# Kernel tuning notes

Hardware: AMD Instinct MI355X
Metric: run time of the kernel (lower is better)

## Reference

```python
import jax, jax.numpy as jnp
import numpy as np

L, B, S, D, H, DK, F = 6, 4, 2048, 512, 8, 64, 2048


def setup_inputs() -> dict:
    key = jax.random.key(0)
    ks = iter(jax.random.split(key, 40))
    def rn(shape, scale=0.02):
        return jax.random.normal(next(ks), shape, jnp.float32) * scale
    inp = {
        "x": jax.random.normal(next(ks), (B, S, D), jnp.float32),
        "enc": jax.random.normal(next(ks), (B, S, D), jnp.float32),
    }
    for pre in ("sa", "ca"):
        inp[f"{pre}_wq"] = rn((L, D, H * DK)); inp[f"{pre}_bq"] = jnp.zeros((L, H * DK), jnp.float32)
        inp[f"{pre}_wk"] = rn((L, D, H * DK)); inp[f"{pre}_bk"] = jnp.zeros((L, H * DK), jnp.float32)
        inp[f"{pre}_wv"] = rn((L, D, H * DK)); inp[f"{pre}_bv"] = jnp.zeros((L, H * DK), jnp.float32)
        inp[f"{pre}_wo"] = rn((L, H * DK, D)); inp[f"{pre}_bo"] = jnp.zeros((L, D), jnp.float32)
    for i in (1, 2, 3):
        inp[f"ln{i}_g"] = jnp.ones((L, D), jnp.float32)
        inp[f"ln{i}_b"] = jnp.zeros((L, D), jnp.float32)
    inp["ff_w1"] = rn((L, D, F)); inp["ff_b1"] = jnp.zeros((L, F), jnp.float32)
    inp["ff_w2"] = rn((L, F, D)); inp["ff_b2"] = jnp.zeros((L, D), jnp.float32)
    return inp


def _layer_norm(z, g, b, eps=1e-5):
    m = z.mean(-1, keepdims=True)
    v = z.var(-1, keepdims=True)
    return (z - m) * jax.lax.rsqrt(v + eps) * g + b


def _mha(q_in, kv_in, wq, bq, wk, bk, wv, bv, wo, bo, causal_bias):
    b, s, _ = q_in.shape
    Q = (q_in @ wq + bq).reshape(b, s, H, DK)   # [B,S,H,DK]
    K = (kv_in @ wk + bk).reshape(b, s, H, DK)
    V = (kv_in @ wv + bv).reshape(b, s, H, DK)
    scores = jnp.einsum("bqhd,bkhd->bhqk", Q, K) / jnp.float32(DK) ** 0.5
    if causal_bias is not None:
        scores = scores + causal_bias  # additive -inf above diagonal
    w = jax.nn.softmax(scores, axis=-1)
    att = jnp.einsum("bhqk,bkhd->bqhd", w, V).reshape(b, s, H * DK)
    return att @ wo + bo


def reference(x, enc, sa_wq, sa_bq, sa_wk, sa_bk, sa_wv, sa_bv, sa_wo, sa_bo,
              ca_wq, ca_bq, ca_wk, ca_bk, ca_wv, ca_bv, ca_wo, ca_bo,
              ln1_g, ln1_b, ln2_g, ln2_b, ln3_g, ln3_b,
              ff_w1, ff_b1, ff_w2, ff_b2):
    s = x.shape[1]
    causal_bias = jnp.triu(jnp.full((s, s), -jnp.inf, jnp.float32), 1)

    params = (sa_wq, sa_bq, sa_wk, sa_bk, sa_wv, sa_bv, sa_wo, sa_bo,
              ca_wq, ca_bq, ca_wk, ca_bk, ca_wv, ca_bv, ca_wo, ca_bo,
              ln1_g, ln1_b, ln2_g, ln2_b, ln3_g, ln3_b,
              ff_w1, ff_b1, ff_w2, ff_b2)

    def block(h, p):
        (swq, sbq, swk, sbk, swv, sbv, swo, sbo,
         cwq, cbq, cwk, cbk, cwv, cbv, cwo, cbo,
         g1, b1, g2, b2, g3, b3, w1, bb1, w2, bb2) = p
        # masked self-attention + residual + LN  (faithful to source)
        x1 = _layer_norm(h + _mha(h, h, swq, sbq, swk, sbk, swv, sbv, swo, sbo, causal_bias), g1, b1)
        # cross-attention; residual comes from the BLOCK INPUT h (source bug kept)
        y = _layer_norm(h + _mha(x1, enc, cwq, cbq, cwk, cbk, cwv, cbv, cwo, cbo, None), g2, b2)
        # FFN; residual from x1 (source bug kept)
        out = _layer_norm(x1 + (jax.nn.relu(y @ w1 + bb1) @ w2 + bb2), g3, b3)
        return out, None

    out, _ = jax.lax.scan(block, x, params)
    return out
```

## Files before the change

### kernel.cpp

```cpp
#include <hip/hip_runtime.h>
#include <stdint.h>

#define LCOUNT 6
#define BB 4
#define SS 2048
#define DD 512
#define HH 8
#define DKK 64
#define FFDIM 2048
#define MM (BB*SS)

typedef __attribute__((ext_vector_type(8))) __bf16 bf16x8;
typedef __attribute__((ext_vector_type(4))) float f32x4;
typedef unsigned short u16;
typedef unsigned long long u64;

__device__ __forceinline__ u16 f2bf(float f) {
  union { __bf16 h; u16 u; } v; v.h = (__bf16)f; return v.u;
}
__device__ __forceinline__ float bf2f(u16 u) {
  union { uint32_t u; float f; } v; v.u = ((uint32_t)u) << 16;
  return v.f;
}

__device__ __forceinline__ void gload_lds16(const u16* gsrc, u16* ldst) {
  __builtin_amdgcn_global_load_lds((const __attribute__((address_space(1))) char*)gsrc,
                                   (__attribute__((address_space(3))) char*)ldst, 16, 0, 0);
}

__global__ __launch_bounds__(256) void f2bf_kernel(const float* __restrict__ in,
                                                   u16* __restrict__ outp, int n) {
  int i = (blockIdx.x * 256 + threadIdx.x) * 8;
  if (i >= n) return;
  float4 a = *(const float4*)&in[i];
  float4 b = *(const float4*)&in[i + 4];
  union { u16 us[8]; uint4 v; } pk;
  pk.us[0] = f2bf(a.x); pk.us[1] = f2bf(a.y); pk.us[2] = f2bf(a.z); pk.us[3] = f2bf(a.w);
  pk.us[4] = f2bf(b.x); pk.us[5] = f2bf(b.y); pk.us[6] = f2bf(b.z); pk.us[7] = f2bf(b.w);
  *(uint4*)&outp[i] = pk.v;
}

__global__ __launch_bounds__(256) void bias_cat(const float* a, const float* b, const float* c,
                                                float* dst, int n, int total) {
  int i = blockIdx.x * 256 + threadIdx.x;
  if (i >= total) return;
  int parts = (c != nullptr) ? 3 : 2;
  int per = parts * n;
  int l = i / per, cc = i % per;
  const float* s = cc < n ? a : (cc < 2 * n ? b : c);
  dst[i] = s[l * n + (cc % n)];
}

__global__ __launch_bounds__(256) void wtrans(const float* __restrict__ W,
                                              u16* __restrict__ Wt, int K_, int N_,
                                              size_t lstride) {
  __shared__ float tile[64 * 65];
  const int l = blockIdx.z;
  const float* Wl = W + (size_t)l * K_ * N_;
  u16* Wtl = Wt + (size_t)l * lstride;
  const int n0 = blockIdx.x * 64, k0 = blockIdx.y * 64;
  const int tid = threadIdx.x;
  const int r = tid >> 2, c4 = (tid & 3) * 16;
#pragma unroll
  for (int j = 0; j < 16; j += 4) {
    float4 v = *(const float4*)&Wl[(size_t)(k0 + r) * N_ + n0 + c4 + j];
    tile[r * 65 + c4 + j + 0] = v.x;
    tile[r * 65 + c4 + j + 1] = v.y;
    tile[r * 65 + c4 + j + 2] = v.z;
    tile[r * 65 + c4 + j + 3] = v.w;
  }
  __syncthreads();
  const int nr = tid >> 2, kc = (tid & 3) * 16;
#pragma unroll
  for (int half = 0; half < 2; ++half) {
    union { u16 us[8]; uint4 v; } pk;
#pragma unroll
    for (int e = 0; e < 8; ++e) pk.us[e] = f2bf(tile[(kc + half * 8 + e) * 65 + nr]);
    *(uint4*)&Wtl[(size_t)(n0 + nr) * K_ + k0 + kc + half * 8] = pk.v;
  }
}

template <int BMT, int BNT, int BKT, bool RELU, bool VT>
__global__ __launch_bounds__(256)
void gemm_bt(const u16* __restrict__ A, const u16* __restrict__ Bt,
             const float* __restrict__ bias, u16* __restrict__ C,
             int N_, int K_, int CS, u16* __restrict__ vt, int vtc0) {
  constexpr int MR = BMT / 32;
  constexpr int NR = BNT / 32;
  constexpr int CH = BKT / 8;
  constexpr int RPR = 2048 / BKT;
  constexpr int KS = BKT / 32;
  __shared__ u16 As[BMT * BKT];
  __shared__ u16 Bs[BNT * BKT];
  const int tid = threadIdx.x;
  const int wid = tid >> 6, lane = tid & 63;
  const int l15 = lane & 15, g = lane >> 4;
  const int wr = wid >> 1, wc = wid & 1;
  const int lrow = (CH == 8) ? (lane >> 3) : (lane >> 4);
  const int lch  = lane & (CH - 1);
  const int wrows = 64 / CH;
  const int lin = blockIdx.x + gridDim.x * blockIdx.y;
  const int nwg = gridDim.x * gridDim.y;
  const int swz = (lin & 7) * (nwg >> 3) + (lin >> 3);
  const int brow = (swz / gridDim.x) * BMT;
  const int bcol = (swz % gridDim.x) * BNT;

  f32x4 acc[MR][NR];
#pragma unroll
  for (int m = 0; m < MR; ++m)
#pragma unroll
    for (int n = 0; n < NR; ++n) acc[m][n] = (f32x4){0.f, 0.f, 0.f, 0.f};

  for (int kt = 0; kt < K_; kt += BKT) {
#pragma unroll
    for (int r = 0; r < BMT / RPR; ++r) {
      int row = r * RPR + wid * wrows + lrow;
      int slot = lch ^ (row & 7);
      gload_lds16(A + (size_t)(brow + row) * K_ + kt + slot * 8,
                  &As[r * 2048 + wid * 512]);
    }
#pragma unroll
    for (int r = 0; r < BNT / RPR; ++r) {
      int row = r * RPR + wid * wrows + lrow;
      int slot = lch ^ (row & 7);
      gload_lds16(Bt + (size_t)(bcol + row) * K_ + kt + slot * 8,
                  &Bs[r * 2048 + wid * 512]);
    }
    __syncthreads();
#pragma unroll
    for (int ks = 0; ks < KS; ++ks) {
      bf16x8 af[MR], bfr[NR];
#pragma unroll
      for (int m = 0; m < MR; ++m) {
        int row = wr * (BMT / 2) + m * 16 + l15;
        int slot = (ks * 4 + g) ^ (row & 7);
        af[m] = *(const bf16x8*)&As[row * BKT + slot * 8];
      }
#pragma unroll
      for (int n = 0; n < NR; ++n) {
        int row = wc * (BNT / 2) + n * 16 + l15;
        int slot = (ks * 4 + g) ^ (row & 7);
        bfr[n] = *(const bf16x8*)&Bs[row * BKT + slot * 8];
      }
#pragma unroll
      for (int m = 0; m < MR; ++m)
#pragma unroll
        for (int n = 0; n < NR; ++n)
          acc[m][n] = __builtin_amdgcn_mfma_f32_16x16x32_bf16(af[m], bfr[n], acc[m][n], 0, 0, 0);
    }
    __syncthreads();
  }
#pragma unroll
  for (int n = 0; n < NR; ++n) {
    int col = bcol + wc * (BNT / 2) + n * 16 + l15;
    float bv = bias ? bias[col] : 0.f;
    if (VT && col >= vtc0) {
      int hh = (col - vtc0) >> 6, dd = (col - vtc0) & 63;
#pragma unroll
      for (int m = 0; m < MR; ++m) {
        int s0g = brow + wr * (BMT / 2) + m * 16 + g * 4;
        int bb = s0g >> 11, ss = s0g & (SS - 1);
        union { u16 us[4]; uint2 v; } pk;
#pragma unroll
        for (int r = 0; r < 4; ++r) pk.us[r] = f2bf(acc[m][n][r] + bv);
        *(uint2*)&vt[(((size_t)(bb * HH + hh)) * DKK + dd) * SS + ss] = pk.v;
      }
    } else {
#pragma unroll
      for (int m = 0; m < MR; ++m) {
#pragma unroll
        for (int r = 0; r < 4; ++r) {
          int rowg = brow + wr * (BMT / 2) + m * 16 + g * 4 + r;
          float v = acc[m][n][r] + bv;
          if (RELU) v = fmaxf(v, 0.f);
          C[(size_t)rowg * CS + col] = f2bf(v);
        }
      }
    }
  }
}

template <bool CAUSAL>
__global__ __launch_bounds__(256, 4)
void attn_kernel(const u16* __restrict__ Qm, const u16* __restrict__ Km,
                 const u16* __restrict__ Vt, u16* __restrict__ Om, int qks) {
  __shared__ u16 Ks[2][64 * 64];
  __shared__ u16 Vs[2][64 * 64];
  const int lin = blockIdx.x;
  const int bh = (lin & 7) * 4 + ((lin >> 3) >> 5);
  const int qc = (lin >> 3) & 31;
  const int qb = (qc & 1) ? (31 - (qc >> 1)) : (qc >> 1);
  const int h = bh & 7, b = bh >> 3;
  const int tid = threadIdx.x, wid = tid >> 6, lane = tid & 63;
  const int l15 = lane & 15, g = lane >> 4;
  const int qstart = qb * 64;
  const size_t qbase = ((size_t)b * SS) * qks + h * DKK;
  const size_t vtbase = (size_t)(b * HH + h) * DKK * SS;
  const size_t obase = ((size_t)b * SS) * DD + h * DKK;
  const int srow = wid * 8 + (lane >> 3);
  const int sslot = lane & 7;
  const int qg = qstart + wid * 16 + l15;
  const float SC = 0.18033688f;
  const int sA = ((2 * g) & 3) * 16 + l15;
  const int sB = ((2 * g + 1) & 3) * 16 + l15;

  const u16* kp = Km + qbase;
  const u16* vp = Vt + vtbase;

  bf16x8 qf[2];
#pragma unroll
  for (int ks = 0; ks < 2; ++ks)
    qf[ks] = *(const bf16x8*)&Qm[qbase + (size_t)qg * qks + ks * 32 + g * 8];

  f32x4 oacc[4];
#pragma unroll
  for (int nb = 0; nb < 4; ++nb) oacc[nb] = (f32x4){0.f, 0.f, 0.f, 0.f};
  float m_run = -3.0e38f, l_run = 0.f;

  const int T = CAUSAL ? (qb + 1) : (SS / 64);

#pragma unroll
  for (int r = 0; r < 2; ++r) {
    int row = r * 32 + srow;
    int slot = sslot ^ (row & 7);
    gload_lds16(kp + (size_t)row * qks + slot * 8, &Ks[0][r * 2048 + wid * 512]);
    gload_lds16(vp + (size_t)row * SS + slot * 8, &Vs[0][r * 2048 + wid * 512]);
  }
  __syncthreads();

  int cur = 0;
  for (int t = 0; t < T; ++t) {
    const int kstart = t * 64;
    if (t + 1 < T) {
#pragma unroll
      for (int r = 0; r < 2; ++r) {
        int row = r * 32 + srow;
        int slot = sslot ^ (row & 7);
        gload_lds16(kp + (size_t)(kstart + 64 + row) * qks + slot * 8,
                    &Ks[cur ^ 1][r * 2048 + wid * 512]);
        gload_lds16(vp + (size_t)row * SS + kstart + 64 + slot * 8,
                    &Vs[cur ^ 1][r * 2048 + wid * 512]);
      }
    }
    f32x4 sacc[4];
#pragma unroll
    for (int nb = 0; nb < 4; ++nb) sacc[nb] = (f32x4){0.f, 0.f, 0.f, 0.f};
    __builtin_amdgcn_s_setprio(1);
#pragma unroll
    for (int nb = 0; nb < 4; ++nb) {
      int row = nb * 16 + l15;
#pragma unroll
      for (int ks = 0; ks < 2; ++ks) {
        bf16x8 kf = *(const bf16x8*)&Ks[cur][row * 64 + (((ks * 4 + g) ^ (row & 7)) * 8)];
        sacc[nb] = __builtin_amdgcn_mfma_f32_16x16x32_bf16(kf, qf[ks], sacc[nb], 0, 0, 0);
      }
    }
    __builtin_amdgcn_s_setprio(0);
    if (CAUSAL && t == T - 1) {
#pragma unroll
      for (int nb = 0; nb < 4; ++nb)
#pragma unroll
        for (int r = 0; r < 4; ++r)
          if ((kstart + nb * 16 + g * 4 + r) > qg) sacc[nb][r] = -3.0e38f;
    }
    f32x4 m4 = sacc[0];
#pragma unroll
    for (int nb = 1; nb < 4; ++nb) {
      m4[0] = fmaxf(m4[0], sacc[nb][0]); m4[1] = fmaxf(m4[1], sacc[nb][1]);
      m4[2] = fmaxf(m4[2], sacc[nb][2]); m4[3] = fmaxf(m4[3], sacc[nb][3]);
    }
    float mx = fmaxf(fmaxf(m4[0], m4[1]), fmaxf(m4[2], m4[3]));
    mx = fmaxf(mx, __shfl_xor(mx, 16));
    mx = fmaxf(mx, __shfl_xor(mx, 32));
    const bool skip = __all(mx <= m_run + 64.0f);
    float mnew = skip ? m_run : fmaxf(m_run, mx);
    float mc = mnew * SC;
    float s = 0.f;
#pragma unroll
    for (int nb = 0; nb < 4; ++nb) {
#pragma unroll
      for (int r = 0; r < 4; ++r) {
        float e = __builtin_amdgcn_exp2f(sacc[nb][r] * SC - mc);
        sacc[nb][r] = e; s += e;
      }
    }
    s += __shfl_xor(s, 16);
    s += __shfl_xor(s, 32);
    if (skip) {
      l_run += s;
    } else {
      float resc = __builtin_amdgcn_exp2f((m_run - mnew) * SC);
      l_run = l_run * resc + s;
      m_run = mnew;
      float ro[4];
#pragma unroll
      for (int r = 0; r < 4; ++r) ro[r] = __shfl(resc, g * 4 + r);
#pragma unroll
      for (int nb = 0; nb < 4; ++nb)
#pragma unroll
        for (int r = 0; r < 4; ++r) oacc[nb][r] *= ro[r];
    }
    u64 pk[4];
#pragma unroll
    for (int nb = 0; nb < 4; ++nb) {
      union { u16 us[4]; u64 v; } z;
#pragma unroll
      for (int r = 0; r < 4; ++r) z.us[r] = f2bf(sacc[nb][r]);
      pk[nb] = z.v;
    }
    bf16x8 pf[2];
#pragma unroll
    for (int ks = 0; ks < 2; ++ks) {
      u64 a0 = __shfl(pk[2 * ks], sA);
      u64 a1 = __shfl(pk[2 * ks + 1], sA);
      u64 b0 = __shfl(pk[2 * ks], sB);
      u64 b1 = __shfl(pk[2 * ks + 1], sB);
      union { u64 q[2]; bf16x8 v; } mrg;
      mrg.q[0] = (g < 2) ? a0 : a1;
      mrg.q[1] = (g < 2) ? b0 : b1;
      pf[ks] = mrg.v;
    }
    __builtin_amdgcn_s_setprio(1);
#pragma unroll
    for (int nb = 0; nb < 4; ++nb) {
      int row = nb * 16 + l15;
#pragma unroll
      for (int ks = 0; ks < 2; ++ks) {
        bf16x8 vf = *(const bf16x8*)&Vs[cur][row * 64 + (((ks * 4 + g) ^ (row & 7)) * 8)];
        oacc[nb] = __builtin_amdgcn_mfma_f32_16x16x32_bf16(pf[ks], vf, oacc[nb], 0, 0, 0);
      }
    }
    __builtin_amdgcn_s_setprio(0);
    __syncthreads();
    cur ^= 1;
  }
  float linv = 1.f / l_run;
  float io[4];
#pragma unroll
  for (int r = 0; r < 4; ++r) io[r] = __shfl(linv, g * 4 + r);
#pragma unroll
  for (int nb = 0; nb < 4; ++nb) {
#pragma unroll
    for (int r = 0; r < 4; ++r) {
      Om[obase + (size_t)(qstart + wid * 16 + g * 4 + r) * DD + nb * 16 + l15] =
          f2bf(oacc[nb][r] * io[r]);
    }
  }
}

__global__ __launch_bounds__(256)
void ln_kernel(const u16* __restrict__ A, const u16* __restrict__ Bv,
               const float* __restrict__ gamma, const float* __restrict__ beta,
               u16* __restrict__ out_bf, float* __restrict__ out_f32) {
  const int row = blockIdx.x * 4 + (threadIdx.x >> 6);
  const int lane = threadIdx.x & 63;
  uint4 av = *(const uint4*)&A[(size_t)row * DD + lane * 8];
  uint4 bv = *(const uint4*)&Bv[(size_t)row * DD + lane * 8];
  const u16* au = (const u16*)&av;
  const u16* bu = (const u16*)&bv;
  float z[8], s = 0.f, s2 = 0.f;
#pragma unroll
  for (int j = 0; j < 8; ++j) {
    float x = bf2f(au[j]) + bf2f(bu[j]);
    z[j] = x; s += x; s2 += x * x;
  }
#pragma unroll
  for (int off = 1; off < 64; off <<= 1) {
    s += __shfl_xor(s, off);
    s2 += __shfl_xor(s2, off);
  }
  float mean = s * (1.f / 512.f);
  float var = s2 * (1.f / 512.f) - mean * mean;
  float rs = rsqrtf(var + 1e-5f);
  union { u16 us[8]; uint4 v; } pk;
#pragma unroll
  for (int j = 0; j < 8; ++j) {
    float o = (z[j] - mean) * rs * gamma[lane * 8 + j] + beta[lane * 8 + j];
    pk.us[j] = f2bf(o);
    if (out_f32) out_f32[(size_t)row * DD + lane * 8 + j] = o;
  }
  *(uint4*)&out_bf[(size_t)row * DD + lane * 8] = pk.v;
}

extern "C" void kernel_launch(void* const* d_in, const int* in_sizes, int n_in,
                              void* d_out, int out_size, void* d_ws, size_t ws_size,
                              hipStream_t stream) {
  const float* x   = (const float*)d_in[0];
  const float* enc = (const float*)d_in[1];
  const float* sa_w[4] = {(const float*)d_in[2], (const float*)d_in[4], (const float*)d_in[6], (const float*)d_in[8]};
  const float* sa_b[4] = {(const float*)d_in[3], (const float*)d_in[5], (const float*)d_in[7], (const float*)d_in[9]};
  const float* ca_w[4] = {(const float*)d_in[10], (const float*)d_in[12], (const float*)d_in[14], (const float*)d_in[16]};
  const float* ca_b[4] = {(const float*)d_in[11], (const float*)d_in[13], (const float*)d_in[15], (const float*)d_in[17]};
  const float* ln_g[3] = {(const float*)d_in[18], (const float*)d_in[20], (const float*)d_in[22]};
  const float* ln_b[3] = {(const float*)d_in[19], (const float*)d_in[21], (const float*)d_in[23]};
  const float* ffw1 = (const float*)d_in[24];
  const float* ffb1 = (const float*)d_in[25];
  const float* ffw2 = (const float*)d_in[26];
  const float* ffb2 = (const float*)d_in[27];

  char* ws = (char*)d_ws;
  size_t o = 0;
  auto take = [&](size_t bytes) {
    void* p = ws + o;
    o += (bytes + 255) & ~(size_t)255;
    return p;
  };
  u16* wqkv  = (u16*)take((size_t)LCOUNT * 1536 * 512 * 2);
  u16* wqca  = (u16*)take((size_t)LCOUNT * 512 * 512 * 2);
  u16* wkvca = (u16*)take((size_t)LCOUNT * 1024 * 512 * 2);
  u16* wosa  = (u16*)take((size_t)LCOUNT * 512 * 512 * 2);
  u16* woca  = (u16*)take((size_t)LCOUNT * 512 * 512 * 2);
  u16* w1t   = (u16*)take((size_t)LCOUNT * 512 * 2048 * 2);
  u16* w2t   = (u16*)take((size_t)LCOUNT * 2048 * 512 * 2);
  float* bqkv = (float*)take((size_t)LCOUNT * 1536 * 4);
  float* bkv  = (float*)take((size_t)LCOUNT * 1024 * 4);
  u16* Hb   = (u16*)take((size_t)MM * 512 * 2);
  u16* Eb   = (u16*)take((size_t)MM * 512 * 2);
  u16* QKVb = (u16*)take((size_t)MM * 1536 * 2);
  u16* Ab   = (u16*)take((size_t)MM * 512 * 2);
  u16* Pb   = (u16*)take((size_t)MM * 512 * 2);
  u16* X1b  = (u16*)take((size_t)MM * 512 * 2);
  u16* Yb   = (u16*)take((size_t)MM * 512 * 2);
  u16* Fb   = (u16*)take((size_t)MM * 2048 * 2);
  u16* Vtb  = Fb;

  f2bf_kernel<<<2048, 256, 0, stream>>>(x, Hb, MM * 512);
  f2bf_kernel<<<2048, 256, 0, stream>>>(enc, Eb, MM * 512);
  wtrans<<<dim3(8, 8, LCOUNT), 256, 0, stream>>>(sa_w[0], wqkv,              512, 512, (size_t)1536 * 512);
  wtrans<<<dim3(8, 8, LCOUNT), 256, 0, stream>>>(sa_w[1], wqkv + 512 * 512,  512, 512, (size_t)1536 * 512);
  wtrans<<<dim3(8, 8, LCOUNT), 256, 0, stream>>>(sa_w[2], wqkv + 1024 * 512, 512, 512, (size_t)1536 * 512);
  wtrans<<<dim3(8, 8, LCOUNT), 256, 0, stream>>>(sa_w[3], wosa,              512, 512, (size_t)512 * 512);
  wtrans<<<dim3(8, 8, LCOUNT), 256, 0, stream>>>(ca_w[0], wqca,              512, 512, (size_t)512 * 512);
  wtrans<<<dim3(8, 8, LCOUNT), 256, 0, stream>>>(ca_w[1], wkvca,             512, 512, (size_t)1024 * 512);
  wtrans<<<dim3(8, 8, LCOUNT), 256, 0, stream>>>(ca_w[2], wkvca + 512 * 512, 512, 512, (size_t)1024 * 512);
  wtrans<<<dim3(8, 8, LCOUNT), 256, 0, stream>>>(ca_w[3], woca,              512, 512, (size_t)512 * 512);
  wtrans<<<dim3(32, 8, LCOUNT), 256, 0, stream>>>(ffw1, w1t, 512, 2048, (size_t)2048 * 512);
  wtrans<<<dim3(8, 32, LCOUNT), 256, 0, stream>>>(ffw2, w2t, 2048, 512, (size_t)512 * 2048);
  bias_cat<<<36, 256, 0, stream>>>(sa_b[0], sa_b[1], sa_b[2], bqkv, 512, LCOUNT * 1536);
  bias_cat<<<24, 256, 0, stream>>>(ca_b[1], ca_b[2], nullptr, bkv, 512, LCOUNT * 1024);

  for (int l = 0; l < LCOUNT; ++l) {
    const size_t w512 = (size_t)l * 512 * 512;
    const size_t wff = (size_t)l * 512 * 2048;
    gemm_bt<128, 128, 64, false, true><<<dim3(12, 64), 256, 0, stream>>>(
        Hb, wqkv + (size_t)l * 1536 * 512, bqkv + l * 1536, QKVb, 1536, 512, 1536, Vtb, 1024);
    attn_kernel<true><<<dim3(1024), 256, 0, stream>>>(QKVb, QKVb + 512, Vtb, Ab, 1536);
    gemm_bt<64, 64, 128, false, false><<<dim3(8, 128), 256, 0, stream>>>(
        Ab, wosa + w512, sa_b[3] + l * 512, Pb, 512, 512, 512, nullptr, 0);
    ln_kernel<<<MM / 4, 256, 0, stream>>>(Hb, Pb, ln_g[0] + l * 512, ln_b[0] + l * 512, X1b, nullptr);
    gemm_bt<64, 64, 128, false, false><<<dim3(8, 128), 256, 0, stream>>>(
        X1b, wqca + w512, ca_b[0] + l * 512, QKVb, 512, 512, 1536, nullptr, 0);
    gemm_bt<128, 128, 64, false, true><<<dim3(8, 64), 256, 0, stream>>>(
        Eb, wkvca + (size_t)l * 1024 * 512, bkv + l * 1024, QKVb + 512, 1024, 512, 1536, Vtb, 512);
    attn_kernel<false><<<dim3(1024), 256, 0, stream>>>(QKVb, QKVb + 512, Vtb, Ab, 1536);
    gemm_bt<64, 64, 128, false, false><<<dim3(8, 128), 256, 0, stream>>>(
        Ab, woca + w512, ca_b[3] + l * 512, Pb, 512, 512, 512, nullptr, 0);
    ln_kernel<<<MM / 4, 256, 0, stream>>>(Hb, Pb, ln_g[1] + l * 512, ln_b[1] + l * 512, Yb, nullptr);
    gemm_bt<128, 128, 64, true, false><<<dim3(16, 64), 256, 0, stream>>>(
        Yb, w1t + wff, ffb1 + l * 2048, Fb, 2048, 512, 2048, nullptr, 0);
    gemm_bt<64, 64, 128, false, false><<<dim3(8, 128), 256, 0, stream>>>(
        Fb, w2t + wff, ffb2 + l * 512, Pb, 512, 2048, 512, nullptr, 0);
    ln_kernel<<<MM / 4, 256, 0, stream>>>(X1b, Pb, ln_g[2] + l * 512, ln_b[2] + l * 512, Hb,
                                          (l == LCOUNT - 1) ? (float*)d_out : nullptr);
  }
}
```

Baseline: 2.040 ms.

## Fuse cross-attn Q/KV GEMMs, batch weight transposes, LDS P-relayout, wider N tiles

Cross-attention Q and KV projections become one 1536-wide GEMM launch, where column blocks at or past 512 read the encoder activations through a second A pointer. The eight 512x512 weight transposes are batched into a single launch. In attention, the P-matrix relayout now goes through a per-wave LDS scratch buffer instead of shuffles. The N=512 output GEMMs move from 64x64 to 64x128 tiles. Together these cut launch count and shuffle cost, at the price of extra LDS use in attention and fewer workgroups for the output GEMMs.

```diff
diff --git a/kernel.cpp b/kernel.cpp
--- a/kernel.cpp
+++ b/kernel.cpp
@@ -13,7 +13,6 @@
 typedef __attribute__((ext_vector_type(8))) __bf16 bf16x8;
 typedef __attribute__((ext_vector_type(4))) float f32x4;
 typedef unsigned short u16;
-typedef unsigned long long u64;
 
 __device__ __forceinline__ u16 f2bf(float f) {
   union { __bf16 h; u16 u; } v; v.h = (__bf16)f; return v.u;
@@ -80,11 +79,45 @@
   }
 }
 
+struct WtBatch {
+  const float* src[8];
+  u16* dst[8];
+  unsigned long long lstr[8];
+};
+__global__ __launch_bounds__(256) void wtrans8(WtBatch wb) {
+  __shared__ float tile[64 * 65];
+  const int z = blockIdx.z;
+  const int slot = z / 6, l = z - slot * 6;
+  const float* Wl = wb.src[slot] + (size_t)l * 512 * 512;
+  u16* Wtl = wb.dst[slot] + (size_t)l * wb.lstr[slot];
+  const int n0 = blockIdx.x * 64, k0 = blockIdx.y * 64;
+  const int tid = threadIdx.x;
+  const int r = tid >> 2, c4 = (tid & 3) * 16;
+#pragma unroll
+  for (int j = 0; j < 16; j += 4) {
+    float4 v = *(const float4*)&Wl[(size_t)(k0 + r) * 512 + n0 + c4 + j];
+    tile[r * 65 + c4 + j + 0] = v.x;
+    tile[r * 65 + c4 + j + 1] = v.y;
+    tile[r * 65 + c4 + j + 2] = v.z;
+    tile[r * 65 + c4 + j + 3] = v.w;
+  }
+  __syncthreads();
+  const int nr = tid >> 2, kc = (tid & 3) * 16;
+#pragma unroll
+  for (int half = 0; half < 2; ++half) {
+    union { u16 us[8]; uint4 v; } pk;
+#pragma unroll
+    for (int e = 0; e < 8; ++e) pk.us[e] = f2bf(tile[(kc + half * 8 + e) * 65 + nr]);
+    *(uint4*)&Wtl[(size_t)(n0 + nr) * 512 + k0 + kc + half * 8] = pk.v;
+  }
+}
+
 template <int BMT, int BNT, int BKT, bool RELU, bool VT>
 __global__ __launch_bounds__(256)
 void gemm_bt(const u16* __restrict__ A, const u16* __restrict__ Bt,
              const float* __restrict__ bias, u16* __restrict__ C,
-             int N_, int K_, int CS, u16* __restrict__ vt, int vtc0) {
+             int N_, int K_, int CS, u16* __restrict__ vt, int vtc0,
+             const u16* __restrict__ A2, int a2col) {
   constexpr int MR = BMT / 32;
   constexpr int NR = BNT / 32;
   constexpr int CH = BKT / 8;
@@ -104,6 +137,7 @@
   const int swz = (lin & 7) * (nwg >> 3) + (lin >> 3);
   const int brow = (swz / gridDim.x) * BMT;
   const int bcol = (swz % gridDim.x) * BNT;
+  const u16* Ap = (A2 != nullptr && bcol >= a2col) ? A2 : A;
 
   f32x4 acc[MR][NR];
 #pragma unroll
@@ -116,7 +150,7 @@
     for (int r = 0; r < BMT / RPR; ++r) {
       int row = r * RPR + wid * wrows + lrow;
       int slot = lch ^ (row & 7);
-      gload_lds16(A + (size_t)(brow + row) * K_ + kt + slot * 8,
+      gload_lds16(Ap + (size_t)(brow + row) * K_ + kt + slot * 8,
                   &As[r * 2048 + wid * 512]);
     }
 #pragma unroll
@@ -186,6 +220,7 @@
                  const u16* __restrict__ Vt, u16* __restrict__ Om, int qks) {
   __shared__ u16 Ks[2][64 * 64];
   __shared__ u16 Vs[2][64 * 64];
+  __shared__ u16 Ps[4][16 * 64];
   const int lin = blockIdx.x;
   const int bh = (lin & 7) * 4 + ((lin >> 3) >> 5);
   const int qc = (lin >> 3) & 31;
@@ -197,12 +232,12 @@
   const size_t qbase = ((size_t)b * SS) * qks + h * DKK;
   const size_t vtbase = (size_t)(b * HH + h) * DKK * SS;
   const size_t obase = ((size_t)b * SS) * DD + h * DKK;
+  u16* psw = &Ps[wid][0];
   const int srow = wid * 8 + (lane >> 3);
   const int sslot = lane & 7;
   const int qg = qstart + wid * 16 + l15;
+  const int pswz = (l15 & 7) << 1;
   const float SC = 0.18033688f;
-  const int sA = ((2 * g) & 3) * 16 + l15;
-  const int sB = ((2 * g + 1) & 3) * 16 + l15;
 
   const u16* kp = Km + qbase;
   const u16* vp = Vt + vtbase;
@@ -300,25 +335,19 @@
 #pragma unroll
         for (int r = 0; r < 4; ++r) oacc[nb][r] *= ro[r];
     }
-    u64 pk[4];
 #pragma unroll
     for (int nb = 0; nb < 4; ++nb) {
-      union { u16 us[4]; u64 v; } z;
-#pragma unroll
-      for (int r = 0; r < 4; ++r) z.us[r] = f2bf(sacc[nb][r]);
-      pk[nb] = z.v;
+      union { u16 us[4]; uint2 v; } pk;
+#pragma unroll
+      for (int r = 0; r < 4; ++r) pk.us[r] = f2bf(sacc[nb][r]);
+      int cp = (nb * 4 + g) ^ pswz;
+      *(uint2*)&psw[l15 * 64 + cp * 4] = pk.v;
     }
     bf16x8 pf[2];
 #pragma unroll
     for (int ks = 0; ks < 2; ++ks) {
-      u64 a0 = __shfl(pk[2 * ks], sA);
-      u64 a1 = __shfl(pk[2 * ks + 1], sA);
-      u64 b0 = __shfl(pk[2 * ks], sB);
-      u64 b1 = __shfl(pk[2 * ks + 1], sB);
-      union { u64 q[2]; bf16x8 v; } mrg;
-      mrg.q[0] = (g < 2) ? a0 : a1;
-      mrg.q[1] = (g < 2) ? b0 : b1;
-      pf[ks] = mrg.v;
+      int cp0 = (8 * ks + 2 * g) ^ pswz;
+      pf[ks] = *(const bf16x8*)&psw[l15 * 64 + cp0 * 4];
     }
     __builtin_amdgcn_s_setprio(1);
 #pragma unroll
@@ -406,14 +435,13 @@
     return p;
   };
   u16* wqkv  = (u16*)take((size_t)LCOUNT * 1536 * 512 * 2);
-  u16* wqca  = (u16*)take((size_t)LCOUNT * 512 * 512 * 2);
-  u16* wkvca = (u16*)take((size_t)LCOUNT * 1024 * 512 * 2);
+  u16* wca   = (u16*)take((size_t)LCOUNT * 1536 * 512 * 2);
   u16* wosa  = (u16*)take((size_t)LCOUNT * 512 * 512 * 2);
   u16* woca  = (u16*)take((size_t)LCOUNT * 512 * 512 * 2);
   u16* w1t   = (u16*)take((size_t)LCOUNT * 512 * 2048 * 2);
   u16* w2t   = (u16*)take((size_t)LCOUNT * 2048 * 512 * 2);
   float* bqkv = (float*)take((size_t)LCOUNT * 1536 * 4);
-  float* bkv  = (float*)take((size_t)LCOUNT * 1024 * 4);
+  float* bca  = (float*)take((size_t)LCOUNT * 1536 * 4);
   u16* Hb   = (u16*)take((size_t)MM * 512 * 2);
   u16* Eb   = (u16*)take((size_t)MM * 512 * 2);
   u16* QKVb = (u16*)take((size_t)MM * 1536 * 2);
@@ -426,40 +454,42 @@
 
   f2bf_kernel<<<2048, 256, 0, stream>>>(x, Hb, MM * 512);
   f2bf_kernel<<<2048, 256, 0, stream>>>(enc, Eb, MM * 512);
-  wtrans<<<dim3(8, 8, LCOUNT), 256, 0, stream>>>(sa_w[0], wqkv,              512, 512, (size_t)1536 * 512);
-  wtrans<<<dim3(8, 8, LCOUNT), 256, 0, stream>>>(sa_w[1], wqkv + 512 * 512,  512, 512, (size_t)1536 * 512);
-  wtrans<<<dim3(8, 8, LCOUNT), 256, 0, stream>>>(sa_w[2], wqkv + 1024 * 512, 512, 512, (size_t)1536 * 512);
-  wtrans<<<dim3(8, 8, LCOUNT), 256, 0, stream>>>(sa_w[3], wosa,              512, 512, (size_t)512 * 512);
-  wtrans<<<dim3(8, 8, LCOUNT), 256, 0, stream>>>(ca_w[0], wqca,              512, 512, (size_t)512 * 512);
-  wtrans<<<dim3(8, 8, LCOUNT), 256, 0, stream>>>(ca_w[1], wkvca,             512, 512, (size_t)1024 * 512);
-  wtrans<<<dim3(8, 8, LCOUNT), 256, 0, stream>>>(ca_w[2], wkvca + 512 * 512, 512, 512, (size_t)1024 * 512);
-  wtrans<<<dim3(8, 8, LCOUNT), 256, 0, stream>>>(ca_w[3], woca,              512, 512, (size_t)512 * 512);
+  WtBatch wb;
+  wb.src[0] = sa_w[0]; wb.dst[0] = wqkv;              wb.lstr[0] = (size_t)1536 * 512;
+  wb.src[1] = sa_w[1]; wb.dst[1] = wqkv + 512 * 512;  wb.lstr[1] = (size_t)1536 * 512;
+  wb.src[2] = sa_w[2]; wb.dst[2] = wqkv + 1024 * 512; wb.lstr[2] = (size_t)1536 * 512;
+  wb.src[3] = sa_w[3]; wb.dst[3] = wosa;              wb.lstr[3] = (size_t)512 * 512;
+  wb.src[4] = ca_w[0]; wb.dst[4] = wca;               wb.lstr[4] = (size_t)1536 * 512;
+  wb.src[5] = ca_w[1]; wb.dst[5] = wca + 512 * 512;   wb.lstr[5] = (size_t)1536 * 512;
+  wb.src[6] = ca_w[2]; wb.dst[6] = wca + 1024 * 512;  wb.lstr[6] = (size_t)1536 * 512;
+  wb.src[7] = ca_w[3]; wb.dst[7] = woca;              wb.lstr[7] = (size_t)512 * 512;
+  wtrans8<<<dim3(8, 8, 48), 256, 0, stream>>>(wb);
   wtrans<<<dim3(32, 8, LCOUNT), 256, 0, stream>>>(ffw1, w1t, 512, 2048, (size_t)2048 * 512);
   wtrans<<<dim3(8, 32, LCOUNT), 256, 0, stream>>>(ffw2, w2t, 2048, 512, (size_t)512 * 2048);
   bias_cat<<<36, 256, 0, stream>>>(sa_b[0], sa_b[1], sa_b[2], bqkv, 512, LCOUNT * 1536);
-  bias_cat<<<24, 256, 0, stream>>>(ca_b[1], ca_b[2], nullptr, bkv, 512, LCOUNT * 1024);
+  bias_cat<<<36, 256, 0, stream>>>(ca_b[0], ca_b[1], ca_b[2], bca, 512, LCOUNT * 1536);
 
   for (int l = 0; l < LCOUNT; ++l) {
     const size_t w512 = (size_t)l * 512 * 512;
     const size_t wff = (size_t)l * 512 * 2048;
     gemm_bt<128, 128, 64, false, true><<<dim3(12, 64), 256, 0, stream>>>(
-        Hb, wqkv + (size_t)l * 1536 * 512, bqkv + l * 1536, QKVb, 1536, 512, 1536, Vtb, 1024);
+        Hb, wqkv + (size_t)l * 1536 * 512, bqkv + l * 1536, QKVb, 1536, 512, 1536, Vtb, 1024,
+        nullptr, 0);
     attn_kernel<true><<<dim3(1024), 256, 0, stream>>>(QKVb, QKVb + 512, Vtb, Ab, 1536);
-    gemm_bt<64, 64, 128, false, false><<<dim3(8, 128), 256, 0, stream>>>(
-        Ab, wosa + w512, sa_b[3] + l * 512, Pb, 512, 512, 512, nullptr, 0);
+    gemm_bt<64, 128, 128, false, false><<<dim3(4, 128), 256, 0, stream>>>(
+        Ab, wosa + w512, sa_b[3] + l * 512, Pb, 512, 512, 512, nullptr, 0, nullptr, 0);
     ln_kernel<<<MM / 4, 256, 0, stream>>>(Hb, Pb, ln_g[0] + l * 512, ln_b[0] + l * 512, X1b, nullptr);
-    gemm_bt<64, 64, 128, false, false><<<dim3(8, 128), 256, 0, stream>>>(
-        X1b, wqca + w512, ca_b[0] + l * 512, QKVb, 512, 512, 1536, nullptr, 0);
-    gemm_bt<128, 128, 64, false, true><<<dim3(8, 64), 256, 0, stream>>>(
-        Eb, wkvca + (size_t)l * 1024 * 512, bkv + l * 1024, QKVb + 512, 1024, 512, 1536, Vtb, 512);
+    gemm_bt<128, 128, 64, false, true><<<dim3(12, 64), 256, 0, stream>>>(
+        X1b, wca + (size_t)l * 1536 * 512, bca + l * 1536, QKVb, 1536, 512, 1536, Vtb, 1024,
+        Eb, 512);
     attn_kernel<false><<<dim3(1024), 256, 0, stream>>>(QKVb, QKVb + 512, Vtb, Ab, 1536);
-    gemm_bt<64, 64, 128, false, false><<<dim3(8, 128), 256, 0, stream>>>(
-        Ab, woca + w512, ca_b[3] + l * 512, Pb, 512, 512, 512, nullptr, 0);
+    gemm_bt<64, 128, 128, false, false><<<dim3(4, 128), 256, 0, stream>>>(
+        Ab, woca + w512, ca_b[3] + l * 512, Pb, 512, 512, 512, nullptr, 0, nullptr, 0);
     ln_kernel<<<MM / 4, 256, 0, stream>>>(Hb, Pb, ln_g[1] + l * 512, ln_b[1] + l * 512, Yb, nullptr);
     gemm_bt<128, 128, 64, true, false><<<dim3(16, 64), 256, 0, stream>>>(
-        Yb, w1t + wff, ffb1 + l * 2048, Fb, 2048, 512, 2048, nullptr, 0);
-    gemm_bt<64, 64, 128, false, false><<<dim3(8, 128), 256, 0, stream>>>(
-        Fb, w2t + wff, ffb2 + l * 512, Pb, 512, 2048, 512, nullptr, 0);
+        Yb, w1t + wff, ffb1 + l * 2048, Fb, 2048, 512, 2048, nullptr, 0, nullptr, 0);
+    gemm_bt<64, 128, 128, false, false><<<dim3(4, 128), 256, 0, stream>>>(
+        Fb, w2t + wff, ffb2 + l * 512, Pb, 512, 2048, 512, nullptr, 0, nullptr, 0);
     ln_kernel<<<MM / 4, 256, 0, stream>>>(X1b, Pb, ln_g[2] + l * 512, ln_b[2] + l * 512, Hb,
                                           (l == LCOUNT - 1) ? (float*)d_out : nullptr);
   }
```

Measured after the change: 1.797 ms. -11.9%, faster.
